# Kernel tuning notes

Hardware: AMD Instinct MI355X
Metric: run time of the kernel (lower is better)

The kernel has to match this reference:

```python
import jax, jax.numpy as jnp
import numpy as np

K, N, D, M, M_RF, N_RF = 512, 512, 16, 64, 16, 64


def cmul(a, b):
    # complex matmul with stacked real/imag in axis -3: a [...,2,m,k], b [...,2,k,n]
    ar, ai = a[..., 0, :, :], a[..., 1, :, :]
    br, bi = b[..., 0, :, :], b[..., 1, :, :]
    return jnp.stack([ar @ br - ai @ bi, ar @ bi + ai @ br], axis=-3)


def conjT(a):
    # complex conjugate transpose
    ar, ai = a[..., 0, :, :], a[..., 1, :, :]
    return jnp.stack([jnp.swapaxes(ar, -1, -2), -jnp.swapaxes(ai, -1, -2)], axis=-3)


def cinv(a):
    # inverse of complex matrix a=[2,n,n] via real 2n x 2n block matrix
    ar, ai = a[0], a[1]
    n = ar.shape[0]
    Mblk = jnp.block([[ar, -ai], [ai, ar]])
    Minv = jnp.linalg.inv(Mblk)
    return jnp.stack([Minv[:n, :n], Minv[n:, :n]], axis=0)


def setup_inputs() -> dict:
    key = jax.random.key(0)
    ks = jax.random.split(key, 8)
    s = 0.05  # keep accumulated products well-scaled
    H = s * jax.random.normal(ks[0], (K, 2, M, N), jnp.float32)
    U_RF = s * jax.random.normal(ks[1], (K, 2, M, M_RF), jnp.float32)
    U_BB = s * jax.random.normal(ks[2], (K, 2, M_RF, D), jnp.float32)
    W = s * jax.random.normal(ks[3], (K, 2, D, D), jnp.float32)
    V_RF = s * jax.random.normal(ks[4], (2, N, N_RF), jnp.float32)
    V_BB = s * jax.random.normal(ks[5], (K, 2, N_RF, D), jnp.float32)
    Y = s * jax.random.normal(ks[6], (K, 2, N, D), jnp.float32)
    rho = jnp.ones((1,), jnp.float32)  # forward arg, unused by the module
    rho_X_layer = jnp.asarray(6.0, jnp.float32)  # learned scalar
    mu = jnp.asarray(1.0, jnp.float32)           # learned scalar
    params4 = 0.001 * jax.random.normal(ks[7], (K, 2, N, D), jnp.float32)
    return dict(H=H, U_RF=U_RF, U_BB=U_BB, W=W, V_RF=V_RF, V_BB=V_BB, Y=Y,
                rho=rho, rho_X_layer=rho_X_layer, mu=mu, params4=params4)


def reference(H, U_RF, U_BB, W, V_RF, V_BB, Y, rho, rho_X_layer, mu, params4):
    # temp[k] = H[k]^H U_RF[k] U_BB[k] : [K,2,N,d]
    temp = cmul(cmul(conjT(H), U_RF), U_BB)
    TW = cmul(temp, W)  # [K,2,N,d]
    # A_rho = sum_k temp W temp^H + I/(2 rho) : [2,N,N]
    A_rho = cmul(TW, conjT(temp)).sum(axis=0)
    I = jnp.stack([jnp.eye(N, dtype=H.dtype), jnp.zeros((N, N), H.dtype)], axis=0)
    A_rho = A_rho + (1.0 / (2.0 * rho_X_layer)) * I
    # B_rho[k] = temp W + 0.5*(V_RF V_BB[k]/rho - Y[k]) : [K,2,N,d]
    B_rho = TW + 0.5 * ((1.0 / rho_X_layer) * cmul(V_RF, V_BB) - Y)
    A_inv = cinv(A_rho + mu * I)  # [2,N,N]
    X = cmul(A_inv, B_rho) + params4  # [K,2,N,d]
    return X
```

## Files before the change

kernel.cpp:

```cpp
#include <hip/hip_runtime.h>

#define KK 512
#define NN 512
#define DD 16
#define MM 64
#define MRF 16
#define NRF 64

typedef __attribute__((ext_vector_type(8))) short bf16x8;
typedef __attribute__((ext_vector_type(4))) float f32x4;
typedef __attribute__((ext_vector_type(8))) unsigned short u16x8;
typedef __attribute__((ext_vector_type(4))) unsigned short u16x4;

#define MFMA16 __builtin_amdgcn_mfma_f32_16x16x32_bf16

static __device__ __forceinline__ unsigned short f2bf(float x) {
    unsigned int u = __float_as_uint(x);
    u += 0x7fffu + ((u >> 16) & 1u);
    return (unsigned short)(u >> 16);
}
static __device__ __forceinline__ float bf2f(unsigned short b) {
    return __uint_as_float((unsigned int)b << 16);
}
static __device__ __forceinline__ unsigned int pk2(float lo, float hi) {
    return (unsigned int)f2bf(lo) | ((unsigned int)f2bf(hi) << 16);
}

union frag_cast { uint4 u; bf16x8 v; };

__global__ __launch_bounds__(256) void vrfb_kernel(
    const float* __restrict__ V_RF, unsigned short* __restrict__ VRFb)
{
    const int idx = blockIdx.x*256 + threadIdx.x;
    const int n = idx >> 7, j = idx & 127;
    const int p = j >> 6, r = j & 63;
    VRFb[idx] = f2bf(V_RF[((size_t)p*NN + n)*NRF + r]);
}

__global__ __launch_bounds__(256) void small_kernel(
    const float* __restrict__ U_RF, const float* __restrict__ U_BB,
    const float* __restrict__ W, const float* __restrict__ V_BB,
    unsigned int* __restrict__ GT2f)
{
    const int k = blockIdx.x, t = threadIdx.x;
    __shared__ float sUR[2][MM][17];
    __shared__ float sUB[2][MRF][DD], sW[2][DD][DD];
    __shared__ float sVB[2][NRF][17];
    __shared__ float sG[2][MM][17], sGW[2][MM][17];

    const float* uf = U_RF + (size_t)k*2*MM*MRF;
    for (int i = t; i < 2*MM*MRF; i += 256) sUR[i>>10][(i>>4)&63][i&15] = uf[i];
    const float* ub = U_BB + (size_t)k*2*MRF*DD;
    for (int i = t; i < 2*MRF*DD; i += 256) sUB[i>>8][(i>>4)&15][i&15] = ub[i];
    const float* ww = W + (size_t)k*2*DD*DD;
    for (int i = t; i < 2*DD*DD; i += 256) sW[i>>8][(i>>4)&15][i&15] = ww[i];
    const float* vb = V_BB + (size_t)k*2*NRF*DD;
    for (int i = t; i < 2*NRF*DD; i += 256) sVB[i>>10][(i>>4)&63][i&15] = vb[i];
    __syncthreads();

    {
        const int m = t >> 2, dq = (t & 3) * 4;
        float gr[4] = {0,0,0,0}, gi[4] = {0,0,0,0};
#pragma unroll
        for (int r = 0; r < MRF; ++r) {
            const float ur = sUR[0][m][r], ui = sUR[1][m][r];
#pragma unroll
            for (int q = 0; q < 4; ++q) {
                const float br = sUB[0][r][dq+q], bi = sUB[1][r][dq+q];
                gr[q] += ur*br - ui*bi;
                gi[q] += ur*bi + ui*br;
            }
        }
#pragma unroll
        for (int q = 0; q < 4; ++q) { sG[0][m][dq+q] = gr[q]; sG[1][m][dq+q] = gi[q]; }
    }
    __syncthreads();

    {
        const int m = t >> 2, dq = (t & 3) * 4;
        float gwr[4] = {0,0,0,0}, gwi[4] = {0,0,0,0};
#pragma unroll
        for (int dp = 0; dp < DD; ++dp) {
            const float gr = sG[0][m][dp], gi = sG[1][m][dp];
#pragma unroll
            for (int q = 0; q < 4; ++q) {
                const float wr = sW[0][dp][dq+q], wi = sW[1][dp][dq+q];
                gwr[q] += gr*wr - gi*wi;
                gwi[q] += gr*wi + gi*wr;
            }
        }
#pragma unroll
        for (int q = 0; q < 4; ++q) { sGW[0][m][dq+q] = gwr[q]; sGW[1][m][dq+q] = gwi[q]; }
    }
    __syncthreads();

    {
        const int lane64 = t & 63, ks = t >> 6;
        const int c = lane64 & 15, kg = lane64 >> 4;
        const int e2b = ks*16 + kg*4;
        unsigned int* dst = GT2f + (size_t)k*6144 + lane64*96 + ks*24;
#pragma unroll
        for (int s = 0; s < 6; ++s) {
            uint4 o;
#pragma unroll
            for (int j = 0; j < 4; ++j) {
                const int e2 = e2b + j;
                const int sl0 = 2*e2;
                const int m0 = sl0 & 63, hi = sl0 >> 6;
                const int m1 = m0 + 1;
                float v0, v1;
                if (s == 0)      { v0 = hi ? sG[1][m0][c]   : sG[0][m0][c];
                                   v1 = hi ? sG[1][m1][c]   : sG[0][m1][c]; }
                else if (s == 1) { v0 = hi ? -sG[0][m0][c]  : sG[1][m0][c];
                                   v1 = hi ? -sG[0][m1][c]  : sG[1][m1][c]; }
                else if (s == 2) { v0 = hi ? sGW[1][m0][c]  : sGW[0][m0][c];
                                   v1 = hi ? sGW[1][m1][c]  : sGW[0][m1][c]; }
                else if (s == 3) { v0 = hi ? -sGW[0][m0][c] : sGW[1][m0][c];
                                   v1 = hi ? -sGW[0][m1][c] : sGW[1][m1][c]; }
                else if (s == 4) { v0 = hi ? -sVB[1][m0][c] : sVB[0][m0][c];
                                   v1 = hi ? -sVB[1][m1][c] : sVB[0][m1][c]; }
                else             { v0 = hi ? sVB[0][m0][c]  : sVB[1][m0][c];
                                   v1 = hi ? sVB[0][m1][c]  : sVB[1][m1][c]; }
                ((unsigned int*)&o)[j] = pk2(v0, v1);
            }
            *reinterpret_cast<uint4*>(dst + s*4) = o;
        }
    }
}

__global__ __launch_bounds__(512) void prep_main(
    const float* __restrict__ H, const unsigned int* __restrict__ GT2f,
    const unsigned short* __restrict__ VRFb,
    const float* __restrict__ Y, const float* __restrict__ rhoX,
    unsigned short* __restrict__ tempb, unsigned short* __restrict__ TWb,
    unsigned short* __restrict__ Bb)
{
    const int nb = blockIdx.x & 3;
    const int k  = blockIdx.x >> 2;
    const int t  = threadIdx.x;
    const int n0 = nb*128;

    __shared__ unsigned int sHf[128][65];
    __shared__ unsigned int sGf[64*97];

    {
        const unsigned int* g = GT2f + (size_t)k*6144 + t*12;
        unsigned int* d = sGf + (t>>3)*97 + 12*(t&7);
        *reinterpret_cast<uint4*>(d)     = *reinterpret_cast<const uint4*>(g);
        *reinterpret_cast<uint4*>(d + 4) = *reinterpret_cast<const uint4*>(g + 4);
        *reinterpret_cast<uint4*>(d + 8) = *reinterpret_cast<const uint4*>(g + 8);
    }
    const float* Hk = H + (size_t)k*128*NN + n0;
#pragma unroll
    for (int pass = 0; pass < 4; ++pass) {
        const int e2 = pass*16 + (t >> 5);
        const int c4 = (t & 31) * 4;
        const float4 a = *reinterpret_cast<const float4*>(Hk + (size_t)(2*e2  )*NN + c4);
        const float4 b = *reinterpret_cast<const float4*>(Hk + (size_t)(2*e2+1)*NN + c4);
        sHf[c4+0][e2] = pk2(a.x, b.x);
        sHf[c4+1][e2] = pk2(a.y, b.y);
        sHf[c4+2][e2] = pk2(a.z, b.z);
        sHf[c4+3][e2] = pk2(a.w, b.w);
    }

    const int w = t >> 6, lane = t & 63;
    const int c = lane & 15, kg = lane >> 4;
    const float irx = 1.f / rhoX[0];
    const int ncol = w*16 + c;
    const int n = n0 + ncol;

    const size_t o0 = ((size_t)(k*2 + 0)*NN + n)*DD + kg*4;
    const size_t o1 = ((size_t)(k*2 + 1)*NN + n)*DD + kg*4;
    const float4 y0 = *reinterpret_cast<const float4*>(Y + o0);
    const float4 y1 = *reinterpret_cast<const float4*>(Y + o1);

    __syncthreads();

    f32x4 aTr = (f32x4)0.f, aTi = (f32x4)0.f;
    f32x4 aWr = (f32x4)0.f, aWi = (f32x4)0.f;
    f32x4 aVr = (f32x4)0.f, aVi = (f32x4)0.f;

#pragma unroll
    for (int ks = 0; ks < 4; ++ks) {
        const int slot0 = ks*32 + kg*8;
        frag_cast fh, g0, g1, g2, g3, v0, v1;
        fh.u = *reinterpret_cast<const uint4*>(&sHf[ncol][ks*16 + kg*4]);
        const unsigned int* gb = sGf + lane*97 + ks*24;
        g0.u = *reinterpret_cast<const uint4*>(gb);
        g1.u = *reinterpret_cast<const uint4*>(gb + 4);
        g2.u = *reinterpret_cast<const uint4*>(gb + 8);
        g3.u = *reinterpret_cast<const uint4*>(gb + 12);
        v0.u = *reinterpret_cast<const uint4*>(gb + 16);
        v1.u = *reinterpret_cast<const uint4*>(gb + 20);
        const bf16x8 bv = *reinterpret_cast<const bf16x8*>(VRFb + (size_t)n*128 + slot0);

        aTr = MFMA16(g0.v, fh.v, aTr, 0, 0, 0);
        aTi = MFMA16(g1.v, fh.v, aTi, 0, 0, 0);
        aWr = MFMA16(g2.v, fh.v, aWr, 0, 0, 0);
        aWi = MFMA16(g3.v, fh.v, aWi, 0, 0, 0);
        aVr = MFMA16(v0.v, bv, aVr, 0, 0, 0);
        aVi = MFMA16(v1.v, bv, aVi, 0, 0, 0);
    }

    {
        const float y0a[4] = {y0.x, y0.y, y0.z, y0.w};
        const float y1a[4] = {y1.x, y1.y, y1.z, y1.w};
        u16x4 tr_, ti_, wr_, wi_, br_, bi_;
#pragma unroll
        for (int r = 0; r < 4; ++r) {
            tr_[r] = f2bf(aTr[r]);  ti_[r] = f2bf(aTi[r]);
            wr_[r] = f2bf(aWr[r]);  wi_[r] = f2bf(aWi[r]);
            br_[r] = f2bf(aWr[r] + 0.5f*(aVr[r]*irx - y0a[r]));
            bi_[r] = f2bf(aWi[r] + 0.5f*(aVi[r]*irx - y1a[r]));
        }
        *reinterpret_cast<u16x4*>(tempb + o0) = tr_;
        *reinterpret_cast<u16x4*>(tempb + o1) = ti_;
        *reinterpret_cast<u16x4*>(TWb + o0)   = wr_;
        *reinterpret_cast<u16x4*>(TWb + o1)   = wi_;
        *reinterpret_cast<u16x4*>(Bb + o0)    = br_;
        *reinterpret_cast<u16x4*>(Bb + o1)    = bi_;
    }
}

__global__ __launch_bounds__(256) void egemm_kernel(
    const unsigned short* __restrict__ TWb, const unsigned short* __restrict__ tmpb,
    float* __restrict__ Epart)
{
    const int ib = blockIdx.x >> 3;
    const int ks = blockIdx.x & 7;
    const int jb = blockIdx.y;
    const int w    = threadIdx.x >> 6;
    const int lane = threadIdx.x & 63;
    const int m  = lane & 15;
    const int kg = lane >> 4;
    const int iw = ib*64 + (w>>1)*32;
    const int jw = jb*64 + (w&1)*32;
    const int d0  = (kg & 1) * 8;
    const int kof = kg >> 1;

    f32x4 RR[2][2], II[2][2], RI[2][2], IR[2][2];
#pragma unroll
    for (int is = 0; is < 2; ++is)
#pragma unroll
        for (int js = 0; js < 2; ++js) {
            RR[is][js] = (f32x4)0.f; II[is][js] = (f32x4)0.f;
            RI[is][js] = (f32x4)0.f; IR[is][js] = (f32x4)0.f;
        }

#pragma unroll 2
    for (int c = 0; c < 32; ++c) {
        const int chunk = ks*32 + c;
        const int kp = chunk*2 + kof;
        const unsigned short* Ab = TWb  + ((size_t)(kp*2+0)*NN + iw + m)*DD + d0;
        const unsigned short* Bb2 = tmpb + ((size_t)(kp*2+0)*NN + jw + m)*DD + d0;
        bf16x8 ar[2], ai[2], br[2], bi[2];
#pragma unroll
        for (int is = 0; is < 2; ++is) {
            ar[is] = *reinterpret_cast<const bf16x8*>(Ab + (size_t)is*16*DD);
            ai[is] = *reinterpret_cast<const bf16x8*>(Ab + (size_t)NN*DD + (size_t)is*16*DD);
        }
#pragma unroll
        for (int js = 0; js < 2; ++js) {
            br[js] = *reinterpret_cast<const bf16x8*>(Bb2 + (size_t)js*16*DD);
            bi[js] = *reinterpret_cast<const bf16x8*>(Bb2 + (size_t)NN*DD + (size_t)js*16*DD);
        }
#pragma unroll
        for (int is = 0; is < 2; ++is)
#pragma unroll
            for (int js = 0; js < 2; ++js) {
                RR[is][js] = MFMA16(ar[is], br[js], RR[is][js], 0, 0, 0);
                II[is][js] = MFMA16(ai[is], bi[js], II[is][js], 0, 0, 0);
                RI[is][js] = MFMA16(ar[is], bi[js], RI[is][js], 0, 0, 0);
                IR[is][js] = MFMA16(ai[is], br[js], IR[is][js], 0, 0, 0);
            }
    }

    float* Eb = Epart + (size_t)ks*2*NN*NN;
#pragma unroll
    for (int is = 0; is < 2; ++is)
#pragma unroll
        for (int js = 0; js < 2; ++js) {
            const int i = iw + is*16 + kg*4;
            const int jx = jw + js*16 + m;
#pragma unroll
            for (int r = 0; r < 4; ++r) {
                Eb[(size_t)(i+r)*NN + jx]               = RR[is][js][r] + II[is][js][r];
                Eb[(size_t)NN*NN + (size_t)(i+r)*NN + jx] = IR[is][js][r] - RI[is][js][r];
            }
        }
}

__global__ __launch_bounds__(256) void reduceinit_kernel(
    const float* __restrict__ Epart,
    const float* __restrict__ rhoX, const float* __restrict__ mu,
    unsigned short* __restrict__ P, unsigned short* __restrict__ PT,
    unsigned short* __restrict__ T1, unsigned short* __restrict__ T1T)
{
    const size_t idx = (size_t)blockIdx.x*256 + threadIdx.x;
    const float ic = 1.f / (1.f/(2.f*rhoX[0]) + mu[0]);
    const size_t pl = (size_t)2*NN*NN;
    float s = 0.f;
#pragma unroll
    for (int ks = 0; ks < 8; ++ks) s += Epart[(size_t)ks*pl + idx];
    const float mm = s * ic;
    const int p = (int)(idx / ((size_t)NN*NN));
    const size_t rem = idx - (size_t)p*NN*NN;
    const int i = (int)(rem / NN), jx = (int)(rem % NN);
    const unsigned short pv = f2bf(-mm);
    const unsigned short tv = f2bf(((p == 0 && i == jx) ? 1.f : 0.f) - mm);
    const size_t tidx = (size_t)p*NN*NN + (size_t)jx*NN + i;
    P[idx] = pv;  PT[tidx] = pv;
    T1[idx] = tv; T1T[tidx] = tv;
}

template<bool ADD_B, bool WRITE_T>
__global__ __launch_bounds__(256) void mm_kernel(
    const unsigned short* __restrict__ A, const unsigned short* __restrict__ BT,
    unsigned short* __restrict__ D, unsigned short* __restrict__ DT)
{
    const int w    = threadIdx.x >> 6;
    const int lane = threadIdx.x & 63;
    const int m  = lane & 15;
    const int kg = lane >> 4;
    const int i0 = blockIdx.y*32;
    const int j0 = blockIdx.x*32;
    const int iw = (w>>1)*16;
    const int jw = (w&1)*16;

    __shared__ unsigned short sD[2][32][34];

    f32x4 RR = (f32x4)0.f, II = (f32x4)0.f, RI = (f32x4)0.f, IR = (f32x4)0.f;

#pragma unroll 8
    for (int c = 0; c < 16; ++c) {
        const int l0 = c*32 + kg*8;
        const bf16x8 ar = *reinterpret_cast<const bf16x8*>(A  + (size_t)(i0+iw+m)*NN + l0);
        const bf16x8 ai = *reinterpret_cast<const bf16x8*>(A  + (size_t)NN*NN + (size_t)(i0+iw+m)*NN + l0);
        const bf16x8 br = *reinterpret_cast<const bf16x8*>(BT + (size_t)(j0+jw+m)*NN + l0);
        const bf16x8 bi = *reinterpret_cast<const bf16x8*>(BT + (size_t)NN*NN + (size_t)(j0+jw+m)*NN + l0);
        RR = MFMA16(ar, br, RR, 0, 0, 0);
        II = MFMA16(ai, bi, II, 0, 0, 0);
        RI = MFMA16(ar, bi, RI, 0, 0, 0);
        IR = MFMA16(ai, br, IR, 0, 0, 0);
    }
    const int i = i0 + iw + kg*4;
    const int jx = j0 + jw + m;
    float adr[4] = {0.f,0.f,0.f,0.f}, adi[4] = {0.f,0.f,0.f,0.f};
    if (ADD_B) {
        const u16x4 badr = *reinterpret_cast<const u16x4*>(BT + (size_t)jx*NN + i);
        const u16x4 badi = *reinterpret_cast<const u16x4*>(BT + (size_t)NN*NN + (size_t)jx*NN + i);
#pragma unroll
        for (int r = 0; r < 4; ++r) { adr[r] = bf2f(badr[r]); adi[r] = bf2f(badi[r]); }
    }
#pragma unroll
    for (int r = 0; r < 4; ++r) {
        const unsigned short dr_ = f2bf(RR[r] - II[r] + adr[r]);
        const unsigned short di_ = f2bf(RI[r] + IR[r] + adi[r]);
        D[(size_t)(i+r)*NN + jx] = dr_;
        D[(size_t)NN*NN + (size_t)(i+r)*NN + jx] = di_;
        if (WRITE_T) {
            sD[0][iw + kg*4 + r][jw + m] = dr_;
            sD[1][iw + kg*4 + r][jw + m] = di_;
        }
    }
    if (WRITE_T) {
        __syncthreads();
        const int t = threadIdx.x;
        const int r8 = t >> 2, seg = t & 3;
        const int plane = r8 >> 5, jloc = r8 & 31;
        u16x8 v;
#pragma unroll
        for (int e = 0; e < 8; ++e) v[e] = sD[plane][seg*8 + e][jloc];
        *reinterpret_cast<u16x8*>(DT + (size_t)plane*NN*NN +
                                  (size_t)(j0 + jloc)*NN + i0 + seg*8) = v;
    }
}

__global__ __launch_bounds__(256) void final_kernel(
    const unsigned short* __restrict__ Sb, const unsigned short* __restrict__ Bb,
    const float* __restrict__ par4,
    const float* __restrict__ rhoX, const float* __restrict__ mu,
    float* __restrict__ Xout)
{
    const int k0 = blockIdx.x * 2;
    __shared__ __align__(16) unsigned short sBT[2][2][DD][520];

#pragma unroll
    for (int kk = 0; kk < 2; ++kk) {
        const unsigned short* Bk = Bb + (size_t)(k0 + kk)*2*NN*DD;
        for (int q = 0; q < 8; ++q) {
            const int t8 = q*256 + threadIdx.x;
            const u16x8 v = *reinterpret_cast<const u16x8*>(Bk + (size_t)t8*8);
            const int flat = t8*8;
            const int p = flat >> 13, n = (flat >> 4) & 511, dd0 = flat & 15;
#pragma unroll
            for (int jj = 0; jj < 8; ++jj) sBT[kk][p][dd0+jj][n] = v[jj];
        }
    }
    __syncthreads();

    const int w    = threadIdx.x >> 6;
    const int lane = threadIdx.x & 63;
    const int m  = lane & 15;
    const int kg = lane >> 4;
    const int i0 = blockIdx.y*64 + w*16;

    f32x4 RR[2], II[2], RI[2], IR[2];
#pragma unroll
    for (int kk = 0; kk < 2; ++kk) {
        RR[kk] = (f32x4)0.f; II[kk] = (f32x4)0.f;
        RI[kk] = (f32x4)0.f; IR[kk] = (f32x4)0.f;
    }

#pragma unroll 2
    for (int c = 0; c < 16; ++c) {
        const int l0 = c*32 + kg*8;
        const bf16x8 ar = *reinterpret_cast<const bf16x8*>(Sb + (size_t)(i0+m)*NN + l0);
        const bf16x8 ai = *reinterpret_cast<const bf16x8*>(Sb + (size_t)NN*NN + (size_t)(i0+m)*NN + l0);
#pragma unroll
        for (int kk = 0; kk < 2; ++kk) {
            const bf16x8 br = *reinterpret_cast<const bf16x8*>(&sBT[kk][0][m][l0]);
            const bf16x8 bi = *reinterpret_cast<const bf16x8*>(&sBT[kk][1][m][l0]);
            RR[kk] = MFMA16(ar, br, RR[kk], 0, 0, 0);
            II[kk] = MFMA16(ai, bi, II[kk], 0, 0, 0);
            RI[kk] = MFMA16(ar, bi, RI[kk], 0, 0, 0);
            IR[kk] = MFMA16(ai, br, IR[kk], 0, 0, 0);
        }
    }
    const float ic = 1.f / (1.f/(2.f*rhoX[0]) + mu[0]);
#pragma unroll
    for (int kk = 0; kk < 2; ++kk) {
        const int k = k0 + kk;
#pragma unroll
        for (int r = 0; r < 4; ++r) {
            const int i = i0 + kg*4 + r;
            const int d = m;
            const size_t idx0 = ((size_t)(k*2+0)*NN + i)*DD + d;
            const size_t idx1 = ((size_t)(k*2+1)*NN + i)*DD + d;
            Xout[idx0] = (RR[kk][r] - II[kk][r])*ic + par4[idx0];
            Xout[idx1] = (RI[kk][r] + IR[kk][r])*ic + par4[idx1];
        }
    }
}

extern "C" void kernel_launch(void* const* d_in, const int* in_sizes, int n_in,
                              void* d_out, int out_size, void* d_ws, size_t ws_size,
                              hipStream_t stream) {
    const float* H     = (const float*)d_in[0];
    const float* U_RF  = (const float*)d_in[1];
    const float* U_BB  = (const float*)d_in[2];
    const float* W     = (const float*)d_in[3];
    const float* V_RF  = (const float*)d_in[4];
    const float* V_BB  = (const float*)d_in[5];
    const float* Y     = (const float*)d_in[6];
    const float* rhoX  = (const float*)d_in[8];
    const float* mu    = (const float*)d_in[9];
    const float* par4  = (const float*)d_in[10];
    float* Xout = (float*)d_out;

    unsigned short* u = (unsigned short*)d_ws;
    const size_t bigE = (size_t)KK*2*NN*DD;
    const size_t plE  = (size_t)2*NN*NN;
    unsigned short* tempb = u;
    unsigned short* TWb   = tempb + bigE;
    unsigned short* Bb    = TWb + bigE;
    unsigned int*   GT2f  = (unsigned int*)(Bb + bigE);
    unsigned short* VRFb  = (unsigned short*)(GT2f + (size_t)KK*6144);
    unsigned short* Pm    = VRFb + (size_t)NN*128;
    unsigned short* PmT   = Pm  + plE;
    unsigned short* T1    = PmT + plE;
    unsigned short* T1T   = T1  + plE;
    unsigned short* Q     = T1T + plE;
    unsigned short* QT    = Q   + plE;
    unsigned short* R     = QT  + plE;
    unsigned short* RT    = R   + plE;
    unsigned short* T2    = RT  + plE;
    unsigned short* T2T   = T2  + plE;
    unsigned short* T3    = T2T + plE;
    unsigned short* T3T   = T3  + plE;
    unsigned short* R2    = T3T + plE;
    unsigned short* Ss    = R2  + plE;
    float* Epart = (float*)(Ss + plE);

    vrfb_kernel<<<256, 256, 0, stream>>>(V_RF, VRFb);
    small_kernel<<<KK, 256, 0, stream>>>(U_RF, U_BB, W, V_BB, GT2f);
    prep_main<<<KK*4, 512, 0, stream>>>(H, GT2f, VRFb, Y, rhoX,
                                        tempb, TWb, Bb);
    egemm_kernel<<<dim3(64, 8), 256, 0, stream>>>(TWb, tempb, Epart);
    reduceinit_kernel<<<(int)(plE/256), 256, 0, stream>>>(Epart, rhoX, mu,
                                                          Pm, PmT, T1, T1T);
    mm_kernel<false,true ><<<dim3(16,16), 256, 0, stream>>>(Pm, PmT, Q,  QT);
    mm_kernel<true ,true ><<<dim3(16,16), 256, 0, stream>>>(Q,  T1T, T2, T2T);
    mm_kernel<false,true ><<<dim3(16,16), 256, 0, stream>>>(Q,  QT,  R,  RT);
    mm_kernel<true ,true ><<<dim3(16,16), 256, 0, stream>>>(R,  T2T, T3, T3T);
    mm_kernel<false,false><<<dim3(16,16), 256, 0, stream>>>(R,  RT,  R2, nullptr);
    mm_kernel<true ,false><<<dim3(16,16), 256, 0, stream>>>(R2, T3T, Ss, nullptr);
    final_kernel<<<dim3(KK/2, 8), 256, 0, stream>>>(Ss, Bb, par4, rhoX, mu, Xout);
}
```

Before: 226.8 us.

## Read G fragments directly from global in fragment order and drop LDS staging

The G/W/V_BB fragment buffer is rewritten in a lane-contiguous layout (ks, slot, lane), so prep_main can load the MFMA operands straight from global memory with coalesced 16-byte loads instead of staging them through shared memory. The H tile is stored row-major in LDS with vectorized uint4 writes and read back as four scalar loads per fragment. The LDS footprint shrinks and launch_bounds asks for more resident blocks per CU. The trade-off is more global/L2 traffic for G, which is reused across the 8 waves, and scalar LDS reads on the H side.

```diff
diff --git a/kernel.cpp b/kernel.cpp
--- a/kernel.cpp
+++ b/kernel.cpp
@@ -98,7 +98,7 @@
         const int lane64 = t & 63, ks = t >> 6;
         const int c = lane64 & 15, kg = lane64 >> 4;
         const int e2b = ks*16 + kg*4;
-        unsigned int* dst = GT2f + (size_t)k*6144 + lane64*96 + ks*24;
+        unsigned int* dstk = GT2f + (size_t)k*6144 + ks*1536 + lane64*4;
 #pragma unroll
         for (int s = 0; s < 6; ++s) {
             uint4 o;
@@ -123,12 +123,12 @@
                                    v1 = hi ? sVB[0][m1][c]  : sVB[1][m1][c]; }
                 ((unsigned int*)&o)[j] = pk2(v0, v1);
             }
-            *reinterpret_cast<uint4*>(dst + s*4) = o;
-        }
-    }
-}
-
-__global__ __launch_bounds__(512) void prep_main(
+            *reinterpret_cast<uint4*>(dstk + s*256) = o;
+        }
+    }
+}
+
+__global__ __launch_bounds__(512, 8) void prep_main(
     const float* __restrict__ H, const unsigned int* __restrict__ GT2f,
     const unsigned short* __restrict__ VRFb,
     const float* __restrict__ Y, const float* __restrict__ rhoX,
@@ -140,16 +140,8 @@
     const int t  = threadIdx.x;
     const int n0 = nb*128;
 
-    __shared__ unsigned int sHf[128][65];
-    __shared__ unsigned int sGf[64*97];
-
-    {
-        const unsigned int* g = GT2f + (size_t)k*6144 + t*12;
-        unsigned int* d = sGf + (t>>3)*97 + 12*(t&7);
-        *reinterpret_cast<uint4*>(d)     = *reinterpret_cast<const uint4*>(g);
-        *reinterpret_cast<uint4*>(d + 4) = *reinterpret_cast<const uint4*>(g + 4);
-        *reinterpret_cast<uint4*>(d + 8) = *reinterpret_cast<const uint4*>(g + 8);
-    }
+    __shared__ unsigned int sH[64][129];
+
     const float* Hk = H + (size_t)k*128*NN + n0;
 #pragma unroll
     for (int pass = 0; pass < 4; ++pass) {
@@ -157,10 +149,10 @@
         const int c4 = (t & 31) * 4;
         const float4 a = *reinterpret_cast<const float4*>(Hk + (size_t)(2*e2  )*NN + c4);
         const float4 b = *reinterpret_cast<const float4*>(Hk + (size_t)(2*e2+1)*NN + c4);
-        sHf[c4+0][e2] = pk2(a.x, b.x);
-        sHf[c4+1][e2] = pk2(a.y, b.y);
-        sHf[c4+2][e2] = pk2(a.z, b.z);
-        sHf[c4+3][e2] = pk2(a.w, b.w);
+        uint4 d;
+        d.x = pk2(a.x, b.x); d.y = pk2(a.y, b.y);
+        d.z = pk2(a.z, b.z); d.w = pk2(a.w, b.w);
+        *reinterpret_cast<uint4*>(&sH[e2][c4]) = d;
     }
 
     const int w = t >> 6, lane = t & 63;
@@ -180,18 +172,24 @@
     f32x4 aWr = (f32x4)0.f, aWi = (f32x4)0.f;
     f32x4 aVr = (f32x4)0.f, aVi = (f32x4)0.f;
 
+    const unsigned int* gk = GT2f + (size_t)k*6144 + lane*4;
+
 #pragma unroll
     for (int ks = 0; ks < 4; ++ks) {
         const int slot0 = ks*32 + kg*8;
+        const int e2b = ks*16 + kg*4;
         frag_cast fh, g0, g1, g2, g3, v0, v1;
-        fh.u = *reinterpret_cast<const uint4*>(&sHf[ncol][ks*16 + kg*4]);
-        const unsigned int* gb = sGf + lane*97 + ks*24;
+        fh.u.x = sH[e2b+0][ncol];
+        fh.u.y = sH[e2b+1][ncol];
+        fh.u.z = sH[e2b+2][ncol];
+        fh.u.w = sH[e2b+3][ncol];
+        const unsigned int* gb = gk + ks*1536;
         g0.u = *reinterpret_cast<const uint4*>(gb);
-        g1.u = *reinterpret_cast<const uint4*>(gb + 4);
-        g2.u = *reinterpret_cast<const uint4*>(gb + 8);
-        g3.u = *reinterpret_cast<const uint4*>(gb + 12);
-        v0.u = *reinterpret_cast<const uint4*>(gb + 16);
-        v1.u = *reinterpret_cast<const uint4*>(gb + 20);
+        g1.u = *reinterpret_cast<const uint4*>(gb + 256);
+        g2.u = *reinterpret_cast<const uint4*>(gb + 512);
+        g3.u = *reinterpret_cast<const uint4*>(gb + 768);
+        v0.u = *reinterpret_cast<const uint4*>(gb + 1024);
+        v1.u = *reinterpret_cast<const uint4*>(gb + 1280);
         const bf16x8 bv = *reinterpret_cast<const bf16x8*>(VRFb + (size_t)n*128 + slot0);
 
         aTr = MFMA16(g0.v, fh.v, aTr, 0, 0, 0);
```

Measured after the change: 218.7 us. -3.5%, faster.
